# Optimization experiments

Measured on AMD Instinct MI355X. Metric: run time of the kernel, lower is better.

Reference implementation:

```python
import jax, jax.numpy as jnp
import numpy as np
from jax import lax

V, H, B, S, N, E = 32000, 128, 8, 512, 50000, 600000


def lstm(x, W_ih, W_hh, b):
    # x: [B,T,D]; W_ih: [4H,D]; W_hh: [4H,H]; b: [4H] (b_ih+b_hh combined)
    Bsz = x.shape[0]
    Hd = W_hh.shape[1]
    xg = jnp.einsum('btd,gd->btg', x, W_ih) + b  # precompute input gates [B,T,4H]
    h0 = jnp.zeros((Bsz, Hd), x.dtype)
    c0 = jnp.zeros((Bsz, Hd), x.dtype)

    def step(carry, g_t):
        h, c = carry
        g = g_t + h @ W_hh.T
        i, f, gg, o = jnp.split(g, 4, axis=-1)
        i = jax.nn.sigmoid(i)
        f = jax.nn.sigmoid(f)
        gg = jnp.tanh(gg)
        o = jax.nn.sigmoid(o)
        c = f * c + i * gg
        h = o * jnp.tanh(c)
        return (h, c), h

    _, hs = lax.scan(step, (h0, c0), jnp.swapaxes(xg, 0, 1))
    return jnp.swapaxes(hs, 0, 1)  # [B,T,H]


def gcn_conv(x, W, b, src, dst, n_nodes):
    # PyG GCNConv: add self-loops, symmetric normalization, out = A_hat (x W) + b
    h = x @ W.T  # [N,H]
    deg = jax.ops.segment_sum(jnp.ones(src.shape[0], x.dtype), dst, num_segments=n_nodes) + 1.0
    dinv = lax.rsqrt(deg)
    norm = dinv[src] * dinv[dst]  # [E]
    agg = jax.ops.segment_sum(h[src] * norm[:, None], dst, num_segments=n_nodes)
    agg = agg + h * (dinv * dinv)[:, None]  # self-loop contribution
    return agg + b


def setup_inputs() -> dict:
    key = jax.random.key(0)
    ks = jax.random.split(key, 20)
    s = 0.02
    return {
        'json_input': jax.random.randint(ks[0], (B, S), 0, V, dtype=jnp.int32),
        'node_ids': jax.random.randint(ks[1], (N,), 0, V, dtype=jnp.int32),
        'edge_index': jax.random.randint(ks[2], (2, E), 0, N, dtype=jnp.int32),
        'embedding': jax.random.normal(ks[3], (V, H), jnp.float32) * s,
        'W_ih_enc': jax.random.normal(ks[4], (4 * H, H), jnp.float32) * s,
        'W_hh_enc': jax.random.normal(ks[5], (4 * H, H), jnp.float32) * s,
        'b_enc': jnp.zeros((4 * H,), jnp.float32),
        'W1': jax.random.normal(ks[6], (H, H), jnp.float32) * s,
        'b1': jnp.zeros((H,), jnp.float32),
        'W2': jax.random.normal(ks[7], (H, H), jnp.float32) * s,
        'b2': jnp.zeros((H,), jnp.float32),
        'Wf': jax.random.normal(ks[8], (H, 2 * H), jnp.float32) * s,
        'bf': jnp.zeros((H,), jnp.float32),
        'W_ih_dec': jax.random.normal(ks[9], (4 * H, H), jnp.float32) * s,
        'W_hh_dec': jax.random.normal(ks[10], (4 * H, H), jnp.float32) * s,
        'b_dec': jnp.zeros((4 * H,), jnp.float32),
        'Wo': jax.random.normal(ks[11], (V, H), jnp.float32) * s,
        'bo': jnp.zeros((V,), jnp.float32),
    }


def reference(json_input, node_ids, edge_index, embedding, W_ih_enc, W_hh_enc, b_enc,
              W1, b1, W2, b2, Wf, bf, W_ih_dec, W_hh_dec, b_dec, Wo, bo):
    src, dst = edge_index[0], edge_index[1]
    # sequence branch
    json_emb = embedding[json_input]                      # [B,S,H]
    json_encoded = lstm(json_emb, W_ih_enc, W_hh_enc, b_enc)  # [B,S,H]
    # graph branch
    node_x = embedding[node_ids]                          # [N,H]
    x = gcn_conv(node_x, W1, b1, src, dst, node_ids.shape[0])
    x = gcn_conv(x, W2, b2, src, dst, node_ids.shape[0])
    # fusion
    graph_summary = jnp.broadcast_to(x.mean(axis=0, keepdims=True), (json_encoded.shape[0], x.shape[1]))
    combined = jnp.concatenate([json_encoded.mean(axis=1), graph_summary], axis=1)  # [B,2H]
    fused = combined @ Wf.T + bf                          # [B,H]
    fused_seq = jnp.broadcast_to(fused[:, None, :], (fused.shape[0], json_input.shape[1], fused.shape[1]))
    # decode
    decoded = lstm(fused_seq, W_ih_dec, W_hh_dec, b_dec)  # [B,S,H]
    return decoded @ Wo.T + bo                            # [B,S,V]
```

## Files before the change

kernel.cpp:

```cpp
#include <hip/hip_runtime.h>
#include <hip/hip_bf16.h>
#include <stdint.h>

#define VV 32000
#define HH 128
#define BB 8
#define SS 512
#define NNODE 50000
#define NEDGE 600000
#define NWORK 240
#define NOWN 125

typedef __attribute__((ext_vector_type(8))) short s16x8;
typedef __attribute__((ext_vector_type(4))) float f32x4;

__device__ __forceinline__ void workers_barrier(int* bar, int tid) {
  __syncthreads();
  if (tid == 0) {
    int g = __hip_atomic_load(&bar[32], __ATOMIC_ACQUIRE, __HIP_MEMORY_SCOPE_AGENT);
    int old = __hip_atomic_fetch_add(&bar[0], 1, __ATOMIC_ACQ_REL, __HIP_MEMORY_SCOPE_AGENT);
    if (old == NWORK-1) {
      __hip_atomic_store(&bar[0], 0, __ATOMIC_RELAXED, __HIP_MEMORY_SCOPE_AGENT);
      __hip_atomic_store(&bar[32], g+1, __ATOMIC_RELEASE, __HIP_MEMORY_SCOPE_AGENT);
    } else {
      while (__hip_atomic_load(&bar[32], __ATOMIC_ACQUIRE, __HIP_MEMORY_SCOPE_AGENT) == g)
        __builtin_amdgcn_s_sleep(32);
    }
  }
  __syncthreads();
}

__device__ __forceinline__ int ntload_i(const int* p) {
  return __builtin_nontemporal_load(p);
}
__device__ __forceinline__ float ntload_f(const float* p) {
  return __builtin_nontemporal_load(p);
}

__global__ __launch_bounds__(256) void xg_enc_kernel(
    const int* __restrict__ jin, const float* __restrict__ emb,
    const float* __restrict__ Wih, const float* __restrict__ bvec,
    float* __restrict__ xg)
{
  __shared__ __align__(16) float arow[8][128];
  const int tid = threadIdx.x, blk = blockIdx.x;
  {
    int r = tid >> 5, c = (tid & 31) << 2;
    int tok = jin[blk*8 + r];
    *(float4*)&arow[r][c] = *(const float4*)&emb[(size_t)tok*HH + c];
  }
  __syncthreads();
  const int g0 = tid * 2;
  const float* w0 = Wih + (size_t)g0*HH;
  const float* w1 = w0 + HH;
  float acc0[8], acc1[8];
  #pragma unroll
  for (int r=0;r<8;r++){ acc0[r]=0.f; acc1[r]=0.f; }
  for (int k=0;k<HH;k+=4) {
    float4 wa = *(const float4*)&w0[k];
    float4 wb = *(const float4*)&w1[k];
    #pragma unroll
    for (int r=0;r<8;r++) {
      float4 av = *(const float4*)&arow[r][k];
      acc0[r] += av.x*wa.x + av.y*wa.y + av.z*wa.z + av.w*wa.w;
      acc1[r] += av.x*wb.x + av.y*wb.y + av.z*wb.z + av.w*wb.w;
    }
  }
  float bb0 = bvec[g0], bb1 = bvec[g0+1];
  #pragma unroll
  for (int r=0;r<8;r++) {
    size_t row = (size_t)blk*8 + r;
    xg[row*512 + g0]     = acc0[r] + bb0;
    xg[row*512 + g0 + 1] = acc1[r] + bb1;
  }
}

__global__ __launch_bounds__(512) void front_kernel(
    const float* __restrict__ xg, const float* __restrict__ WhhE, float* __restrict__ hmean,
    const float* __restrict__ Wo, __hip_bfloat16* __restrict__ Bhi, __hip_bfloat16* __restrict__ Blo,
    const int* __restrict__ esrc, const int* __restrict__ edst, const int* __restrict__ nids,
    const float* __restrict__ emb,
    float* __restrict__ deg, float* __restrict__ dinv, float* __restrict__ s1,
    float* __restrict__ s2, float* __restrict__ cc, float* __restrict__ ee,
    float* __restrict__ csum, float* __restrict__ gvec,
    const float* __restrict__ W1, const float* __restrict__ b1,
    const float* __restrict__ W2, const float* __restrict__ b2, float* __restrict__ mvec,
    int* bar)
{
  __shared__ __align__(16) char shraw[131072];
  const int bid = blockIdx.x, tid = threadIdx.x;

  if (bid < 8) {
    float* h_s   = (float*)shraw;
    float* act_s = ((float*)shraw) + 128;
    const int b = bid;

    const f32x4* Wrow = (const f32x4*)(WhhE + (size_t)tid*HH);
    f32x4 w[32];
    #pragma unroll
    for (int k=0;k<32;k++) w[k] = Wrow[k];
    #pragma unroll
    for (int k=0;k<32;k++) asm volatile("" : "+v"(w[k]));

    const float* xgrow = xg + (size_t)b*SS*512;
    float xv = xgrow[tid];
    if (tid < 128) h_s[tid] = 0.f;
    float cstate = 0.f, hsum = 0.f;
    __syncthreads();

    for (int t=0;t<SS;t++) {
      int tn = (t < SS-1) ? (t+1) : t;
      float nxv = xgrow[(size_t)tn*512 + tid];
      float a0=0.f,a1=0.f,a2=0.f,a3=0.f;
      #pragma unroll
      for (int k=0;k<32;k++) {
        f32x4 hv = *(const f32x4*)&h_s[k*4];
        a0 += w[k].x*hv.x; a1 += w[k].y*hv.y;
        a2 += w[k].z*hv.z; a3 += w[k].w*hv.w;
      }
      float s = (a0+a1)+(a2+a3) + xv;
      int gid = tid >> 7;
      float act = (gid==2) ? tanhf(s) : 1.0f/(1.0f+expf(-s));
      act_s[tid] = act;
      __syncthreads();
      if (tid < 128) {
        float i_ = act_s[tid], f_ = act_s[128+tid], g_ = act_s[256+tid], o_ = act_s[384+tid];
        cstate = f_*cstate + i_*g_;
        float hh = o_*tanhf(cstate);
        h_s[tid] = hh;
        hsum += hh;
      }
      xv = nxv;
      __syncthreads();
    }
    if (tid < 128) hmean[b*HH + tid] = hsum * (1.0f/512.0f);
  } else {
    const int wbid = bid - 8;
    float* red = (float*)shraw;

    for (int i = wbid*512 + tid; i < VV*HH/4; i += NWORK*512) {
      f32x4 v = __builtin_nontemporal_load((const f32x4*)&Wo[i*4]);
      float vv[4] = {v.x, v.y, v.z, v.w};
      #pragma unroll
      for (int k=0;k<4;k++) {
        __hip_bfloat16 h = __float2bfloat16(vv[k]);
        float rem = vv[k] - __bfloat162float(h);
        __hip_bfloat16 l = __float2bfloat16(rem);
        __builtin_nontemporal_store(*(unsigned short*)&h, (unsigned short*)&Bhi[i*4+k]);
        __builtin_nontemporal_store(*(unsigned short*)&l, (unsigned short*)&Blo[i*4+k]);
      }
    }
    workers_barrier(bar, tid);
    for (int i = wbid*512 + tid; i < NEDGE; i += NWORK*512)
      atomicAdd(&deg[ntload_i(&edst[i])], 1.0f);
    workers_barrier(bar, tid);
    for (int n = wbid*512 + tid; n < NNODE; n += NWORK*512)
      dinv[n] = 1.0f / sqrtf(ntload_f(&deg[n]) + 1.0f);
    workers_barrier(bar, tid);
    for (int i = wbid*512 + tid; i < NEDGE; i += NWORK*512)
      atomicAdd(&s1[ntload_i(&esrc[i])], dinv[ntload_i(&edst[i])]);
    workers_barrier(bar, tid);
    {
      float lsum = 0.f;
      for (int n = wbid*512 + tid; n < NNODE; n += NWORK*512) {
        float d = ntload_f(&dinv[n]); float v = d*ntload_f(&s1[n]) + d*d;
        cc[n] = v; lsum += v;
      }
      red[tid] = lsum; __syncthreads();
      for (int sfl=256; sfl>0; sfl>>=1) { if (tid < sfl) red[tid] += red[tid+sfl]; __syncthreads(); }
      if (tid==0) atomicAdd(csum, red[0]);
    }
    workers_barrier(bar, tid);
    for (int i = wbid*512 + tid; i < NEDGE; i += NWORK*512) {
      int d = ntload_i(&edst[i]);
      atomicAdd(&s2[ntload_i(&esrc[i])], cc[d]*dinv[d]);
    }
    workers_barrier(bar, tid);
    for (int n = wbid*512 + tid; n < NNODE; n += NWORK*512) {
      float d = ntload_f(&dinv[n]);
      ee[n] = d*ntload_f(&s2[n]) + ntload_f(&cc[n])*d*d;
    }
    workers_barrier(bar, tid);
    {
      int j = tid & 127, sub = tid >> 7;
      float acc = 0.f;
      for (int n = wbid*4 + sub; n < NNODE; n += NWORK*4)
        acc += ntload_f(&ee[n]) * ntload_f(&emb[(size_t)ntload_i(&nids[n])*HH + j]);
      red[tid] = acc; __syncthreads();
      if (tid < 128) atomicAdd(&gvec[j], red[tid] + red[tid+128] + red[tid+256] + red[tid+384]);
    }
    workers_barrier(bar, tid);
    if (wbid == 0) {
      float* gs = (float*)shraw;
      float* v1 = gs + 128;
      if (tid < 128) gs[tid] = gvec[tid];
      __syncthreads();
      if (tid < 128) {
        float a = 0.f;
        for (int k=0;k<128;k++) a += gs[k]*W1[tid*128+k];
        v1[tid] = a + csum[0]*b1[tid];
      }
      __syncthreads();
      if (tid < 128) {
        float a2 = 0.f;
        for (int k=0;k<128;k++) a2 += v1[k]*W2[tid*128+k];
        mvec[tid] = a2 * (1.0f/(float)NNODE) + b2[tid];
      }
    }
  }
}

__global__ __launch_bounds__(512) void dec_gemm_kernel(
    const float* __restrict__ hmean, const float* __restrict__ mvec,
    const float* __restrict__ Wf, const float* __restrict__ bfv,
    const float* __restrict__ Wihd, const float* __restrict__ bd,
    const float* __restrict__ Whh,
    __hip_bfloat16* __restrict__ ahi, __hip_bfloat16* __restrict__ alo,
    const __hip_bfloat16* __restrict__ Bhi, const __hip_bfloat16* __restrict__ Blo,
    const float* __restrict__ bo, float* __restrict__ out, int* __restrict__ prog)
{
  __shared__ __align__(16) char shraw[131072];
  const int bid = blockIdx.x, tid = threadIdx.x;

  if (bid < 8) {
    float* h_s   = (float*)shraw;
    float* act_s = ((float*)shraw) + 128;
    float* fus   = (float*)(shraw + 4096);
    const int b = bid;

    const f32x4* Wrow = (const f32x4*)(Whh + (size_t)tid*HH);
    f32x4 w[32];
    #pragma unroll
    for (int k=0;k<32;k++) w[k] = Wrow[k];
    #pragma unroll
    for (int k=0;k<32;k++) asm volatile("" : "+v"(w[k]));

    float* comb = act_s;
    if (tid < 128) comb[tid] = hmean[b*128 + tid];
    else if (tid < 256) comb[tid] = mvec[tid - 128];
    __syncthreads();
    if (tid < 128) {
      float a = 0.f;
      for (int k=0;k<256;k++) a += comb[k]*Wf[tid*256+k];
      fus[tid] = a + bfv[tid];
    }
    __syncthreads();
    float xv;
    {
      float a = 0.f;
      for (int k=0;k<128;k++) a += fus[k]*Wihd[tid*128+k];
      xv = a + bd[tid];
    }
    __syncthreads();
    if (tid < 128) h_s[tid] = 0.f;
    float cstate = 0.f;
    __syncthreads();

    for (int t=0;t<SS;t++) {
      float a0=0.f,a1=0.f,a2=0.f,a3=0.f;
      #pragma unroll
      for (int k=0;k<32;k++) {
        f32x4 hv = *(const f32x4*)&h_s[k*4];
        a0 += w[k].x*hv.x; a1 += w[k].y*hv.y;
        a2 += w[k].z*hv.z; a3 += w[k].w*hv.w;
      }
      float s = (a0+a1)+(a2+a3) + xv;
      int gid = tid >> 7;
      float act = (gid==2) ? tanhf(s) : 1.0f/(1.0f+expf(-s));
      act_s[tid] = act;
      __syncthreads();
      if (tid < 128) {
        float i_ = act_s[tid], f_ = act_s[128+tid], g_ = act_s[256+tid], o_ = act_s[384+tid];
        cstate = f_*cstate + i_*g_;
        float hh = o_*tanhf(cstate);
        h_s[tid] = hh;
        size_t row = (size_t)b*SS + t;
        __hip_bfloat16 hi = __float2bfloat16(hh);
        float rem = hh - __bfloat162float(hi);
        __hip_bfloat16 lo = __float2bfloat16(rem);
        __builtin_nontemporal_store(*(unsigned short*)&hi, (unsigned short*)&ahi[row*HH + tid]);
        __builtin_nontemporal_store(*(unsigned short*)&lo, (unsigned short*)&alo[row*HH + tid]);
      }
      __syncthreads();
      if ((t & 63) == 63) {
        __threadfence();
        __syncthreads();
        if (tid == 0)
          __hip_atomic_store(&prog[b*32], (t >> 6) + 1,
                             __ATOMIC_RELEASE, __HIP_MEMORY_SCOPE_AGENT);
      }
    }
  } else {
    short* smem = (short*)shraw;
    const int nblk = bid - 8;

    const short* bsrc[2] = {
      (const short*)Bhi + (size_t)nblk*256*HH,
      (const short*)Blo + (size_t)nblk*256*HH };
    #pragma unroll
    for (int p=0;p<2;p++) {
      #pragma unroll
      for (int it=0; it<8; it++) {
        int off  = it*8192 + tid*16;
        int row  = off >> 8;
        int soff = off ^ ((row & 15) << 4);
        __builtin_amdgcn_global_load_lds(
          (const __attribute__((address_space(1))) void*)((const char*)bsrc[p] + soff),
          (__attribute__((address_space(3))) void*)((char*)smem + p*65536 + off),
          16, 0, 0);
      }
    }
    __syncthreads();

    const int lane = tid & 63;
    const int wid  = tid >> 6;
    const int wm = wid >> 2, wn = wid & 3;
    const int l15 = lane & 15, l4 = lane >> 4;
    const short* Ah = (const short*)ahi;
    const short* Al = (const short*)alo;

    for (int c = 0; c < 8; ++c) {
      for (int b = 0; b < 8; ++b) {
        if (tid == 0) {
          while (__hip_atomic_load(&prog[b*32], __ATOMIC_ACQUIRE,
                                   __HIP_MEMORY_SCOPE_AGENT) <= c)
            __builtin_amdgcn_s_sleep(64);
        }
        __syncthreads();

        const int mbase = b*512 + c*64 + wm*32;
        f32x4 acc[2][4] = {};
        #pragma unroll
        for (int s=0;s<4;s++) {
          s16x8 bh[4], bl[4], ah[2], al[2];
          #pragma unroll
          for (int qn=0;qn<4;qn++) {
            int rb   = wn*64 + qn*16 + l15;
            int offb = (rb*256 + s*64 + l4*16) ^ ((rb & 15) << 4);
            bh[qn] = *(const s16x8*)((const char*)smem + offb);
            bl[qn] = *(const s16x8*)((const char*)smem + 65536 + offb);
          }
          #pragma unroll
          for (int qm=0;qm<2;qm++) {
            int arow = mbase + qm*16 + l15;
            size_t aoff = (size_t)arow*HH + s*32 + l4*8;
            ah[qm] = *(const s16x8*)(Ah + aoff);
            al[qm] = *(const s16x8*)(Al + aoff);
          }
          #pragma unroll
          for (int qm=0;qm<2;qm++) {
            #pragma unroll
            for (int qn=0;qn<4;qn++) {
              acc[qm][qn] = __builtin_amdgcn_mfma_f32_16x16x32_bf16(bh[qn], ah[qm], acc[qm][qn], 0,0,0);
              acc[qm][qn] = __builtin_amdgcn_mfma_f32_16x16x32_bf16(bl[qn], ah[qm], acc[qm][qn], 0,0,0);
              acc[qm][qn] = __builtin_amdgcn_mfma_f32_16x16x32_bf16(bh[qn], al[qm], acc[qm][qn], 0,0,0);
            }
          }
        }
        #pragma unroll
        for (int qm=0;qm<2;qm++) {
          int row = mbase + qm*16 + l15;
          #pragma unroll
          for (int qn=0;qn<4;qn++) {
            int colb = nblk*256 + wn*64 + qn*16 + l4*4;
            f32x4 bv = *(const f32x4*)&bo[colb];
            f32x4 oo = acc[qm][qn] + bv;
            __builtin_nontemporal_store(oo, (f32x4*)&out[(size_t)row*VV + colb]);
          }
        }
      }
    }
  }
}

extern "C" void kernel_launch(void* const* d_in, const int* in_sizes, int n_in,
                              void* d_out, int out_size, void* d_ws, size_t ws_size,
                              hipStream_t stream)
{
  (void)in_sizes; (void)n_in; (void)out_size; (void)ws_size;
  const int*   jin   = (const int*)d_in[0];
  const int*   nids  = (const int*)d_in[1];
  const int*   esrc  = (const int*)d_in[2];
  const int*   edst  = esrc + NEDGE;
  const float* emb   = (const float*)d_in[3];
  const float* WihE  = (const float*)d_in[4];
  const float* WhhE  = (const float*)d_in[5];
  const float* bE    = (const float*)d_in[6];
  const float* W1    = (const float*)d_in[7];
  const float* b1    = (const float*)d_in[8];
  const float* W2    = (const float*)d_in[9];
  const float* b2    = (const float*)d_in[10];
  const float* Wf    = (const float*)d_in[11];
  const float* bfv   = (const float*)d_in[12];
  const float* WihD  = (const float*)d_in[13];
  const float* WhhD  = (const float*)d_in[14];
  const float* bD    = (const float*)d_in[15];
  const float* Wo    = (const float*)d_in[16];
  const float* bo    = (const float*)d_in[17];
  float* out = (float*)d_out;

  char* ws = (char*)d_ws;
  size_t off = 0;
  auto alloc = [&](size_t bytes) { size_t o = off; off = (off + bytes + 255) & ~(size_t)255; return o; };

  int*   prog = (int*)(ws + alloc(BB*32*4));
  int*   bar  = (int*)(ws + alloc(64*4));
  float* deg  = (float*)(ws + alloc(NNODE*4));
  float* s1   = (float*)(ws + alloc(NNODE*4));
  float* s2   = (float*)(ws + alloc(NNODE*4));
  float* gvec = (float*)(ws + alloc(128*4));
  float* csum = (float*)(ws + alloc(4));
  size_t zero_bytes = off;
  float* dinv = (float*)(ws + alloc(NNODE*4));
  float* cc   = (float*)(ws + alloc(NNODE*4));
  float* ee   = (float*)(ws + alloc(NNODE*4));
  float* mvec = (float*)(ws + alloc(128*4));
  float* hmean= (float*)(ws + alloc(BB*HH*4));
  float* xgenc= (float*)(ws + alloc((size_t)BB*SS*512*4));
  __hip_bfloat16* Ahi = (__hip_bfloat16*)(ws + alloc((size_t)BB*SS*HH*2));
  __hip_bfloat16* Alo = (__hip_bfloat16*)(ws + alloc((size_t)BB*SS*HH*2));
  __hip_bfloat16* Bhi = (__hip_bfloat16*)(ws + alloc((size_t)VV*HH*2));
  __hip_bfloat16* Blo = (__hip_bfloat16*)(ws + alloc((size_t)VV*HH*2));

  hipMemsetAsync(ws, 0, zero_bytes, stream);

  xg_enc_kernel<<<dim3((BB*SS)/8), dim3(256), 0, stream>>>(jin, emb, WihE, bE, xgenc);

  front_kernel<<<dim3(8 + NWORK), dim3(512), 0, stream>>>(
      xgenc, WhhE, hmean, Wo, Bhi, Blo,
      esrc, edst, nids, emb, deg, dinv, s1, s2, cc, ee, csum, gvec,
      W1, b1, W2, b2, mvec, bar);

  dec_gemm_kernel<<<dim3(8 + NOWN), dim3(512), 0, stream>>>(
      hmean, mvec, Wf, bfv, WihD, bD, WhhD,
      Ahi, Alo, Bhi, Blo, bo, out, prog);
}
```

Measured before the change: 1.100 ms.

## Publish decoder progress every 32 steps and halve projection chunk size

The decoder LSTM now signals progress every 32 timesteps instead of every 64, and the output-projection blocks consume 32-row chunks (16 per wave) over 16 chunks. The aim is to shrink the tail after the recurrent decoder finishes, so the vocab projection overlaps it more closely. The worker count for the earlier phases is halved, and the last chunk uses regular stores instead of nontemporal ones. Each MFMA pass now reuses the B fragments across fewer A rows, which lowers arithmetic intensity and adds more synchronisation polls.

```diff
diff --git a/kernel.cpp b/kernel.cpp
--- a/kernel.cpp
+++ b/kernel.cpp
@@ -8,7 +8,7 @@
 #define SS 512
 #define NNODE 50000
 #define NEDGE 600000
-#define NWORK 240
+#define NWORK 120
 #define NOWN 125
 
 typedef __attribute__((ext_vector_type(8))) short s16x8;
@@ -282,11 +282,11 @@
         __builtin_nontemporal_store(*(unsigned short*)&lo, (unsigned short*)&alo[row*HH + tid]);
       }
       __syncthreads();
-      if ((t & 63) == 63) {
+      if ((t & 31) == 31) {
         __threadfence();
         __syncthreads();
         if (tid == 0)
-          __hip_atomic_store(&prog[b*32], (t >> 6) + 1,
+          __hip_atomic_store(&prog[b*32], (t >> 5) + 1,
                              __ATOMIC_RELEASE, __HIP_MEMORY_SCOPE_AGENT);
       }
     }
@@ -319,7 +319,7 @@
     const short* Ah = (const short*)ahi;
     const short* Al = (const short*)alo;
 
-    for (int c = 0; c < 8; ++c) {
+    for (int c = 0; c < 16; ++c) {
       for (int b = 0; b < 8; ++b) {
         if (tid == 0) {
           while (__hip_atomic_load(&prog[b*32], __ATOMIC_ACQUIRE,
@@ -328,11 +328,11 @@
         }
         __syncthreads();
 
-        const int mbase = b*512 + c*64 + wm*32;
-        f32x4 acc[2][4] = {};
+        const int mbase = b*512 + c*32 + wm*16;
+        f32x4 acc[4] = {};
         #pragma unroll
         for (int s=0;s<4;s++) {
-          s16x8 bh[4], bl[4], ah[2], al[2];
+          s16x8 bh[4], bl[4], ah, al;
           #pragma unroll
           for (int qn=0;qn<4;qn++) {
             int rb   = wn*64 + qn*16 + l15;
@@ -340,32 +340,37 @@
             bh[qn] = *(const s16x8*)((const char*)smem + offb);
             bl[qn] = *(const s16x8*)((const char*)smem + 65536 + offb);
           }
-          #pragma unroll
-          for (int qm=0;qm<2;qm++) {
-            int arow = mbase + qm*16 + l15;
+          {
+            int arow = mbase + l15;
             size_t aoff = (size_t)arow*HH + s*32 + l4*8;
-            ah[qm] = *(const s16x8*)(Ah + aoff);
-            al[qm] = *(const s16x8*)(Al + aoff);
+            ah = *(const s16x8*)(Ah + aoff);
+            al = *(const s16x8*)(Al + aoff);
           }
           #pragma unroll
-          for (int qm=0;qm<2;qm++) {
+          for (int qn=0;qn<4;qn++) {
+            acc[qn] = __builtin_amdgcn_mfma_f32_16x16x32_bf16(bh[qn], ah, acc[qn], 0,0,0);
+            acc[qn] = __builtin_amdgcn_mfma_f32_16x16x32_bf16(bl[qn], ah, acc[qn], 0,0,0);
+            acc[qn] = __builtin_amdgcn_mfma_f32_16x16x32_bf16(bh[qn], al, acc[qn], 0,0,0);
+          }
+        }
+        {
+          int row = mbase + l15;
+          if (c == 15) {
             #pragma unroll
             for (int qn=0;qn<4;qn++) {
-              acc[qm][qn] = __builtin_amdgcn_mfma_f32_16x16x32_bf16(bh[qn], ah[qm], acc[qm][qn], 0,0,0);
-              acc[qm][qn] = __builtin_amdgcn_mfma_f32_16x16x32_bf16(bl[qn], ah[qm], acc[qm][qn], 0,0,0);
-              acc[qm][qn] = __builtin_amdgcn_mfma_f32_16x16x32_bf16(bh[qn], al[qm], acc[qm][qn], 0,0,0);
+              int colb = nblk*256 + wn*64 + qn*16 + l4*4;
+              f32x4 bv = *(const f32x4*)&bo[colb];
+              f32x4 oo = acc[qn] + bv;
+              *(f32x4*)&out[(size_t)row*VV + colb] = oo;
             }
-          }
-        }
-        #pragma unroll
-        for (int qm=0;qm<2;qm++) {
-          int row = mbase + qm*16 + l15;
-          #pragma unroll
-          for (int qn=0;qn<4;qn++) {
-            int colb = nblk*256 + wn*64 + qn*16 + l4*4;
-            f32x4 bv = *(const f32x4*)&bo[colb];
-            f32x4 oo = acc[qm][qn] + bv;
-            __builtin_nontemporal_store(oo, (f32x4*)&out[(size_t)row*VV + colb]);
+          } else {
+            #pragma unroll
+            for (int qn=0;qn<4;qn++) {
+              int colb = nblk*256 + wn*64 + qn*16 + l4*4;
+              f32x4 bv = *(const f32x4*)&bo[colb];
+              f32x4 oo = acc[qn] + bv;
+              __builtin_nontemporal_store(oo, (f32x4*)&out[(size_t)row*VV + colb]);
+            }
           }
         }
       }
```

Result: no change. 1.099 ms (-0.1%).
